# Kernel optimization log

Hardware: AMD Instinct MI355X
Metric: run time of the kernel (lower is better)

## Reference

```python
import math
import jax, jax.numpy as jnp
import numpy as np

B, S, D, DK = 4, 2048, 1024, 128


def setup_inputs() -> dict:
    key = jax.random.key(0)
    ks = jax.random.split(key, 9)
    x = jax.random.normal(ks[0], (B, S, D), dtype=jnp.float32)
    # padding at the tail of each sequence (True = padded position)
    lengths = jax.random.randint(ks[1], (B,), S // 2, S)
    padding_mask = jnp.arange(S)[None, :] >= lengths[:, None]  # [B, S] bool
    s = 1.0 / math.sqrt(D)
    Wq = jax.random.normal(ks[2], (D, DK), dtype=jnp.float32) * s
    bq = jnp.zeros((DK,), dtype=jnp.float32)
    Wk = jax.random.normal(ks[3], (D, DK), dtype=jnp.float32) * s
    bk = jnp.zeros((DK,), dtype=jnp.float32)
    Wv = jax.random.normal(ks[4], (D, D), dtype=jnp.float32) * s
    bv = jnp.zeros((D,), dtype=jnp.float32)
    return {"input": x, "padding_mask": padding_mask,
            "Wq": Wq, "bq": bq, "Wk": Wk, "bk": bk, "Wv": Wv, "bv": bv}


def reference(input, padding_mask, Wq, bq, Wk, bk, Wv, bv):
    scale = math.sqrt(DK)
    q = input @ Wq + bq                      # [B, S, DK]
    k = input @ Wk + bk                      # [B, S, DK]
    v = input @ Wv + bv                      # [B, S, D]
    scores = jnp.einsum('bqd,bkd->bqk', q, k) / scale  # [B, S, S]
    causal = jnp.triu(jnp.ones((S, S), dtype=bool), 1)  # True above diagonal
    mask = causal[None, :, :] | padding_mask[:, None, :] | padding_mask[:, :, None]
    scores = jnp.where(mask, -jnp.inf, scores)
    # rows that are fully masked get all-zero logits -> uniform softmax (matches torch edge case)
    all_neg = jnp.all(mask, axis=-1)         # [B, S]
    scores = jnp.where(all_neg[..., None], 0.0, scores)
    attn = jax.nn.softmax(scores, axis=-1)
    return jnp.einsum('bqk,bkd->bqd', attn, v)
```

## Files before the change

kernel.cpp:

```cpp
#include <hip/hip_runtime.h>
#include <cstdint>
#include <cstddef>

#define B_  4
#define S_  2048
#define D_  1024
#define DK_ 128

typedef float  f32x4   __attribute__((ext_vector_type(4)));
typedef short  bf16x8s __attribute__((ext_vector_type(8)));
typedef unsigned int   u32;
typedef unsigned short u16;

__device__ inline u32 rne(float f) {
    u32 u = __builtin_bit_cast(u32, f);
    return (u + 0x7fffu + ((u >> 16) & 1u)) >> 16;
}
__device__ inline u32 pack2(float a, float b) { return rne(a) | (rne(b) << 16); }
__device__ inline bf16x8s ldfrag(const u16* p) {
    union { uint4 u; bf16x8s v; } c;
    c.u = *(const uint4*)p;
    return c.v;
}
__device__ inline f32x4 MM(bf16x8s a, bf16x8s b, f32x4 c) {
    return __builtin_amdgcn_mfma_f32_16x16x32_bf16(a, b, c, 0, 0, 0);
}
__device__ inline void gload_lds16(const void* gsrc, void* ldst) {
    __builtin_amdgcn_global_load_lds(
        (const __attribute__((address_space(1))) unsigned int*)gsrc,
        (__attribute__((address_space(3))) unsigned int*)ldst, 16, 0, 0);
}

__global__ void lengths_kernel(const uint8_t* __restrict__ mask,
                               int* __restrict__ lengths) {
    int b = blockIdx.x;
    bool is_i32 = (mask[S_ - 1] == 0);
    __shared__ int cnt[256];
    int t = threadIdx.x;
    int c = 0;
    for (int i = t; i < S_; i += 256) {
        int val;
        if (is_i32) val = ((const int*)mask)[b * S_ + i];
        else        val = mask[b * S_ + i];
        c += (val == 0) ? 1 : 0;
    }
    cnt[t] = c;
    __syncthreads();
    for (int s = 128; s > 0; s >>= 1) {
        if (t < s) cnt[t] += cnt[t + s];
        __syncthreads();
    }
    if (t == 0) lengths[b] = cnt[0];
}

__global__ __launch_bounds__(256) void tobf16_kernel(
    const float* __restrict__ in, u16* __restrict__ out) {
    size_t i = (size_t)blockIdx.x * 256 + threadIdx.x;
    float4 f = ((const float4*)in)[i];
    ushort4 o = { (u16)rne(f.x), (u16)rne(f.y), (u16)rne(f.z), (u16)rne(f.w) };
    ((ushort4*)out)[i] = o;
}

__global__ __launch_bounds__(256) void transpose_tobf16_kernel(
    const float* __restrict__ W, u16* __restrict__ T, int K, int N) {
    __shared__ float tl[32][33];
    const int t = threadIdx.x, tx = t & 31, ty = t >> 5;
    const int n0 = blockIdx.x * 32, k0 = blockIdx.y * 32;
#pragma unroll
    for (int i = 0; i < 4; ++i)
        tl[ty + i * 8][tx] = W[(size_t)(k0 + ty + i * 8) * N + n0 + tx];
    __syncthreads();
#pragma unroll
    for (int i = 0; i < 4; ++i) {
        float f = tl[tx][ty + i * 8];
        T[(size_t)(n0 + ty + i * 8) * K + k0 + tx] = (u16)rne(f);
    }
}

template<int BM, int BN, int WM, int WN>
__global__ __launch_bounds__(256) void gemm_nt(
    const u16* __restrict__ A, const u16* __restrict__ Bm,
    const float* __restrict__ bias_col, const float* __restrict__ bias_row,
    float scale, u16* __restrict__ C, int N, int K,
    size_t bStride, size_t cStride)
{
    constexpr int FM = WM / 16, FN = WN / 16;
    const int t = threadIdx.x, w = t >> 6, lane = t & 63;
    const int g = lane >> 4, c16 = lane & 15;
    const int m0 = blockIdx.y * BM + (w >> 1) * WM;
    const int n0 = blockIdx.x * BN + (w & 1) * WN;
    Bm += blockIdx.z * bStride;
    C  += blockIdx.z * cStride;

    f32x4 acc[FM][FN];
#pragma unroll
    for (int i = 0; i < FM; ++i)
#pragma unroll
        for (int j = 0; j < FN; ++j) acc[i][j] = (f32x4){0.f, 0.f, 0.f, 0.f};

    size_t aoff[FM], boff[FN];
#pragma unroll
    for (int i = 0; i < FM; ++i) aoff[i] = (size_t)(m0 + i * 16 + c16) * K + g * 8;
#pragma unroll
    for (int j = 0; j < FN; ++j) boff[j] = (size_t)(n0 + j * 16 + c16) * K + g * 8;

#pragma unroll 2
    for (int k0 = 0; k0 < K; k0 += 32) {
        bf16x8s a[FM], b[FN];
#pragma unroll
        for (int i = 0; i < FM; ++i) a[i] = ldfrag(A + aoff[i] + k0);
#pragma unroll
        for (int j = 0; j < FN; ++j) b[j] = ldfrag(Bm + boff[j] + k0);
#pragma unroll
        for (int i = 0; i < FM; ++i)
#pragma unroll
            for (int j = 0; j < FN; ++j)
                acc[i][j] = MM(a[i], b[j], acc[i][j]);
    }

#pragma unroll
    for (int i = 0; i < FM; ++i)
#pragma unroll
        for (int j = 0; j < FN; ++j) {
            const int n = n0 + j * 16 + c16;
            const float bc = bias_col ? bias_col[n] : 0.f;
#pragma unroll
            for (int r = 0; r < 4; ++r) {
                const int m = m0 + i * 16 + g * 4 + r;
                const float br = bias_row ? bias_row[m] : 0.f;
                float val = (acc[i][j][r] + bc + br) * scale;
                C[(size_t)m * N + n] = (u16)rne(val);
            }
        }
}

__global__ __launch_bounds__(64) void vsum_rows_kernel(
    const u16* __restrict__ vt, float* __restrict__ vsumf) {
    const int blk = blockIdx.x;
    const int lane = threadIdx.x;
    const u16* rr = vt + (size_t)blk * S_;
    float s = 0.f;
    for (int ch = lane; ch < S_ / 8; ch += 64) {
        union { uint4 u; u16 e[8]; } a;
        a.u = ((const uint4*)rr)[ch];
#pragma unroll
        for (int j = 0; j < 8; ++j)
            s += __builtin_bit_cast(float, (u32)a.e[j] << 16);
    }
#pragma unroll
    for (int off = 1; off < 64; off <<= 1) s += __shfl_xor(s, off);
    if (lane == 0) vsumf[blk] = s;
}

#define KVB 32

__global__ __launch_bounds__(256, 3) void flash_mfma(
    const u16* __restrict__ qb, const u16* __restrict__ kbuf,
    const u16* __restrict__ vt, const float* __restrict__ vsumf,
    const int* __restrict__ lengths, float* __restrict__ out)
{
    const int lin     = (int)blockIdx.x;
    const int logical = (lin & 7) * 128 + (lin >> 3);
    const int tile    = 31 - (logical & 31);
    const int grp     = logical >> 5;
    const int b       = grp >> 3;
    const int slice   = grp & 7;

    const int r0 = tile * 64;
    const int t = threadIdx.x, w = t >> 6, lane = t & 63;
    const int g = lane >> 4, c16 = lane & 15;
    const int len = lengths[b];

    if (r0 >= len) {
        const float inv = 1.0f / (float)S_;
        const float4* vs4 = (const float4*)(vsumf + (size_t)b * D_ + slice * 128);
        for (int idx = t; idx < 64 * 32; idx += 256) {
            int rr = idx >> 5, c4 = idx & 31;
            float4 vv = vs4[c4];
            float4 o = { vv.x * inv, vv.y * inv, vv.z * inv, vv.w * inv };
            ((float4*)(out + ((size_t)(b * S_ + r0 + rr)) * D_ + slice * 128))[c4] = o;
        }
        return;
    }

    __shared__ alignas(16) u16 ksm[2][KVB * DK_];
    __shared__ alignas(16) u16 vsm[2][128 * KVB];

    const int qr = r0 + w * 16;
    const int qg = qr + c16;

    bf16x8s Q[4];
    {
        const size_t qrow = (size_t)(b * S_ + qr + c16) * DK_;
#pragma unroll
        for (int dt = 0; dt < 4; ++dt)
            Q[dt] = ldfrag(qb + qrow + dt * 32 + g * 8);
    }

    f32x4 acc[8];
#pragma unroll
    for (int i = 0; i < 8; ++i) acc[i] = (f32x4){0.f, 0.f, 0.f, 0.f};
    float m_r = -3.0e38f, l_r = 0.f;

    const int keyloc0 = ((c16 >> 2) << 3) + (c16 & 3);
    const int kmax_w  = (qr >= len) ? -1 : min(qr + 15, len - 1);
    const int kmaxblk = min(r0 + 63, len - 1);
    const int nt      = kmaxblk / KVB + 1;

    auto stage = [&](int bufi, int kb2) {
#pragma unroll
        for (int i = 0; i < 2; ++i) {
            const int slot = i * 256 + w * 64 + lane;
            const int row  = slot >> 4;
            const int segd = (slot & 15) ^ ((row & 3) | (((row >> 3) & 3) << 2));
            const u16* gsrc = kbuf + (size_t)(b * S_ + kb2 + row) * DK_ + segd * 8;
            gload_lds16(gsrc, &ksm[bufi][(size_t)(i * 256 + w * 64) * 8]);
        }
#pragma unroll
        for (int i = 0; i < 2; ++i) {
            const int slot = i * 256 + w * 64 + lane;
            const int row  = slot >> 2;
            const int segd = (slot & 3) ^ ((row >> 1) & 3);
            const u16* gsrc = vt + (size_t)(b * D_ + slice * 128 + row) * S_
                                 + kb2 + segd * 8;
            gload_lds16(gsrc, &vsm[bufi][(size_t)(i * 256 + w * 64) * 8]);
        }
    };

    stage(0, 0);
    __syncthreads();

    for (int ti = 0; ti < nt; ++ti) {
        const int kb  = ti * KVB;
        const int cur = ti & 1;
        if (ti + 1 < nt) stage(cur ^ 1, kb + KVB);

        if (kb <= kmax_w) {
            f32x4 sT[2];
#pragma unroll
            for (int kt = 0; kt < 2; ++kt) {
                f32x4 s = (f32x4){0.f, 0.f, 0.f, 0.f};
#pragma unroll
                for (int dt = 0; dt < 4; ++dt) {
                    const bf16x8s kf = *(const bf16x8s*)&ksm[cur]
                        [(keyloc0 + kt * 4) * DK_ + (((dt * 4 + g) ^ c16) * 8)];
                    s = MM(kf, Q[dt], s);
                }
                sT[kt] = s;
            }
#pragma unroll
            for (int kt = 0; kt < 2; ++kt)
#pragma unroll
                for (int r = 0; r < 4; ++r) {
                    int key = kb + g * 8 + kt * 4 + r;
                    if (key > qg) sT[kt][r] = -3.0e38f;
                }
            float cmax = sT[0][0];
#pragma unroll
            for (int r = 1; r < 4; ++r) cmax = fmaxf(cmax, sT[0][r]);
#pragma unroll
            for (int r = 0; r < 4; ++r) cmax = fmaxf(cmax, sT[1][r]);
            cmax = fmaxf(cmax, __shfl_xor(cmax, 16));
            cmax = fmaxf(cmax, __shfl_xor(cmax, 32));

            const bool noresc = __all(cmax <= m_r + 8.0f);
            float m_new = m_r, sc = 1.0f;
            if (!noresc) {
                m_new = fmaxf(m_r, cmax);
                sc = __expf(m_r - m_new);
            }

            float p[2][4];
            float rs = 0.f;
#pragma unroll
            for (int kt = 0; kt < 2; ++kt)
#pragma unroll
                for (int r = 0; r < 4; ++r) {
                    p[kt][r] = __expf(sT[kt][r] - m_new);
                    rs += p[kt][r];
                }
            rs += __shfl_xor(rs, 16);
            rs += __shfl_xor(rs, 32);

            if (!noresc) {
                float scr0 = __shfl(sc, g * 4 + 0, 16);
                float scr1 = __shfl(sc, g * 4 + 1, 16);
                float scr2 = __shfl(sc, g * 4 + 2, 16);
                float scr3 = __shfl(sc, g * 4 + 3, 16);
                f32x4 scv = { scr0, scr1, scr2, scr3 };
#pragma unroll
                for (int i = 0; i < 8; ++i) acc[i] *= scv;
                l_r = l_r * sc + rs;
                m_r = m_new;
            } else {
                l_r += rs;
            }

            union { u32 wrd[4]; bf16x8s v; } pa;
            pa.wrd[0] = pack2(p[0][0], p[0][1]);
            pa.wrd[1] = pack2(p[0][2], p[0][3]);
            pa.wrd[2] = pack2(p[1][0], p[1][1]);
            pa.wrd[3] = pack2(p[1][2], p[1][3]);

#pragma unroll
            for (int cg = 0; cg < 8; ++cg) {
                const bf16x8s vf = *(const bf16x8s*)&vsm[cur]
                    [(cg * 16 + c16) * KVB + ((g ^ ((c16 >> 1) & 3)) * 8)];
                acc[cg] = MM(pa.v, vf, acc[cg]);
            }
        }

        __syncthreads();
    }

    const float linv = 1.0f / l_r;
    float iv[4];
    bool valid[4];
#pragma unroll
    for (int r = 0; r < 4; ++r) {
        const int row = g * 4 + r;
        iv[r] = __shfl(linv, row, 16);
        valid[r] = (qr + row) < len;
    }
    const float invS = 1.0f / (float)S_;
#pragma unroll
    for (int cg = 0; cg < 8; ++cg) {
        const int d = slice * 128 + cg * 16 + c16;
        const float vsv = vsumf[(size_t)b * D_ + d] * invS;
#pragma unroll
        for (int r = 0; r < 4; ++r) {
            const int rowg = qr + g * 4 + r;
            const float val = valid[r] ? acc[cg][r] * iv[r] : vsv;
            out[((size_t)(b * S_ + rowg)) * D_ + d] = val;
        }
    }
}

extern "C" void kernel_launch(void* const* d_in, const int* in_sizes, int n_in,
                              void* d_out, int out_size, void* d_ws, size_t ws_size,
                              hipStream_t stream) {
    const float*   x    = (const float*)d_in[0];
    const uint8_t* mask = (const uint8_t*)d_in[1];
    const float*   Wq   = (const float*)d_in[2];
    const float*   bq   = (const float*)d_in[3];
    const float*   Wk   = (const float*)d_in[4];
    const float*   bk   = (const float*)d_in[5];
    const float*   Wv   = (const float*)d_in[6];
    const float*   bv   = (const float*)d_in[7];
    float* out = (float*)d_out;

    u16* u = (u16*)d_ws;
    u16* x_bf = u;                    u += (size_t)8192 * 1024;
    u16* wqt  = u;                    u += (size_t)128 * 1024;
    u16* wkt  = u;                    u += (size_t)128 * 1024;
    u16* wvt  = u;                    u += (size_t)1024 * 1024;
    u16* qb   = u;                    u += (size_t)8192 * 128;
    u16* kbuf = u;                    u += (size_t)8192 * 128;
    u16* vt   = u;                    u += (size_t)B_ * 1024 * 2048;
    float* vsumf = (float*)u;
    int* lengths = (int*)(vsumf + B_ * D_);

    const float SCALE = 0.08838834764831845f;

    lengths_kernel<<<dim3(B_), dim3(256), 0, stream>>>(mask, lengths);
    tobf16_kernel<<<dim3(8192), dim3(256), 0, stream>>>(x, x_bf);
    transpose_tobf16_kernel<<<dim3(4, 32), dim3(256), 0, stream>>>(Wq, wqt, 1024, 128);
    transpose_tobf16_kernel<<<dim3(4, 32), dim3(256), 0, stream>>>(Wk, wkt, 1024, 128);
    transpose_tobf16_kernel<<<dim3(32, 32), dim3(256), 0, stream>>>(Wv, wvt, 1024, 1024);

    gemm_nt<64, 64, 32, 32><<<dim3(2, 128, 1), dim3(256), 0, stream>>>(
        x_bf, wqt, bq, nullptr, SCALE, qb, 128, 1024, 0, 0);
    gemm_nt<64, 64, 32, 32><<<dim3(2, 128, 1), dim3(256), 0, stream>>>(
        x_bf, wkt, bk, nullptr, 1.0f, kbuf, 128, 1024, 0, 0);
    gemm_nt<128, 128, 64, 64><<<dim3(16, 8, B_), dim3(256), 0, stream>>>(
        wvt, x_bf, nullptr, bv, 1.0f, vt, 2048, 1024,
        (size_t)2048 * 1024, (size_t)1024 * 2048);

    vsum_rows_kernel<<<dim3(B_ * D_), dim3(64), 0, stream>>>(vt, vsumf);

    flash_mfma<<<dim3(1024), dim3(256), 0, stream>>>(
        qb, kbuf, vt, vsumf, lengths, out);
}
```

Baseline: 304.6 us.

## Stage GEMM tiles through swizzled double-buffered LDS and fuse Q/K projections

Replaces the direct-from-global fragment GEMMs with kernels that stage A and B tiles into double-buffered, XOR-swizzled shared memory using direct global-to-LDS loads, so each tile is reused across waves. The Q and K projections are merged into one GEMM over a concatenated transposed weight, with the epilogue routing columns to the q or k buffer. The goal is to cut redundant global loads and one launch, at the cost of LDS usage and a barrier per k-step.

Result: faster. 244.8 us (-19.7%).

```diff
diff --git a/kernel.cpp b/kernel.cpp
--- a/kernel.cpp
+++ b/kernel.cpp
@@ -77,59 +77,165 @@
     }
 }
 
-template<int BM, int BN, int WM, int WN>
-__global__ __launch_bounds__(256) void gemm_nt(
-    const u16* __restrict__ A, const u16* __restrict__ Bm,
-    const float* __restrict__ bias_col, const float* __restrict__ bias_row,
-    float scale, u16* __restrict__ C, int N, int K,
-    size_t bStride, size_t cStride)
+#define GBK 32
+
+__global__ __launch_bounds__(256, 2) void gemm_lds_vt(
+    const u16* __restrict__ A,
+    const u16* __restrict__ Bm,
+    const float* __restrict__ bias_row,
+    u16* __restrict__ C)
 {
-    constexpr int FM = WM / 16, FN = WN / 16;
+    const int K = 1024, N = 2048;
     const int t = threadIdx.x, w = t >> 6, lane = t & 63;
     const int g = lane >> 4, c16 = lane & 15;
-    const int m0 = blockIdx.y * BM + (w >> 1) * WM;
-    const int n0 = blockIdx.x * BN + (w & 1) * WN;
-    Bm += blockIdx.z * bStride;
-    C  += blockIdx.z * cStride;
-
-    f32x4 acc[FM][FN];
-#pragma unroll
-    for (int i = 0; i < FM; ++i)
-#pragma unroll
-        for (int j = 0; j < FN; ++j) acc[i][j] = (f32x4){0.f, 0.f, 0.f, 0.f};
-
-    size_t aoff[FM], boff[FN];
-#pragma unroll
-    for (int i = 0; i < FM; ++i) aoff[i] = (size_t)(m0 + i * 16 + c16) * K + g * 8;
-#pragma unroll
-    for (int j = 0; j < FN; ++j) boff[j] = (size_t)(n0 + j * 16 + c16) * K + g * 8;
-
-#pragma unroll 2
-    for (int k0 = 0; k0 < K; k0 += 32) {
-        bf16x8s a[FM], b[FN];
-#pragma unroll
-        for (int i = 0; i < FM; ++i) a[i] = ldfrag(A + aoff[i] + k0);
-#pragma unroll
-        for (int j = 0; j < FN; ++j) b[j] = ldfrag(Bm + boff[j] + k0);
-#pragma unroll
-        for (int i = 0; i < FM; ++i)
-#pragma unroll
-            for (int j = 0; j < FN; ++j)
+    const int m0 = blockIdx.y * 128;
+    const int n0 = blockIdx.x * 128;
+    const u16* Bb = Bm + (size_t)blockIdx.z * 2048 * 1024;
+    u16* Cb = C + (size_t)blockIdx.z * 1024 * 2048;
+
+    __shared__ alignas(16) u16 As[2][128 * GBK];
+    __shared__ alignas(16) u16 Bs[2][128 * GBK];
+
+    auto stage = [&](int buf, int k0) {
+#pragma unroll
+        for (int call = 0; call < 2; ++call) {
+            const int slot = call * 256 + w * 64 + lane;
+            const int row  = slot >> 2;
+            const int segd = (slot & 3) ^ ((row >> 1) & 3);
+            gload_lds16(A + (size_t)(m0 + row) * K + k0 + segd * 8,
+                        &As[buf][(size_t)(call * 256 + w * 64) * 8]);
+        }
+#pragma unroll
+        for (int call = 0; call < 2; ++call) {
+            const int slot = call * 256 + w * 64 + lane;
+            const int row  = slot >> 2;
+            const int segd = (slot & 3) ^ ((row >> 1) & 3);
+            gload_lds16(Bb + (size_t)(n0 + row) * K + k0 + segd * 8,
+                        &Bs[buf][(size_t)(call * 256 + w * 64) * 8]);
+        }
+    };
+
+    f32x4 acc[4][4];
+#pragma unroll
+    for (int i = 0; i < 4; ++i)
+#pragma unroll
+        for (int j = 0; j < 4; ++j) acc[i][j] = (f32x4){0.f, 0.f, 0.f, 0.f};
+
+    const int rbase = (w >> 1) * 64;
+    const int cbase = (w & 1) * 64;
+    const int segr  = g ^ ((c16 >> 1) & 3);
+
+    stage(0, 0);
+    __syncthreads();
+    for (int ks = 0; ks < K / GBK; ++ks) {
+        const int cur = ks & 1;
+        if (ks + 1 < K / GBK) stage(cur ^ 1, (ks + 1) * GBK);
+        bf16x8s a[4], b[4];
+#pragma unroll
+        for (int i = 0; i < 4; ++i)
+            a[i] = *(const bf16x8s*)&As[cur][(rbase + i * 16 + c16) * GBK + segr * 8];
+#pragma unroll
+        for (int j = 0; j < 4; ++j)
+            b[j] = *(const bf16x8s*)&Bs[cur][(cbase + j * 16 + c16) * GBK + segr * 8];
+#pragma unroll
+        for (int i = 0; i < 4; ++i)
+#pragma unroll
+            for (int j = 0; j < 4; ++j)
                 acc[i][j] = MM(a[i], b[j], acc[i][j]);
-    }
-
-#pragma unroll
-    for (int i = 0; i < FM; ++i)
-#pragma unroll
-        for (int j = 0; j < FN; ++j) {
-            const int n = n0 + j * 16 + c16;
-            const float bc = bias_col ? bias_col[n] : 0.f;
+        __syncthreads();
+    }
+
+#pragma unroll
+    for (int i = 0; i < 4; ++i)
+#pragma unroll
+        for (int j = 0; j < 4; ++j) {
+            const int n = n0 + cbase + j * 16 + c16;
 #pragma unroll
             for (int r = 0; r < 4; ++r) {
-                const int m = m0 + i * 16 + g * 4 + r;
-                const float br = bias_row ? bias_row[m] : 0.f;
-                float val = (acc[i][j][r] + bc + br) * scale;
-                C[(size_t)m * N + n] = (u16)rne(val);
+                const int m = m0 + rbase + i * 16 + g * 4 + r;
+                Cb[(size_t)m * N + n] = (u16)rne(acc[i][j][r] + bias_row[m]);
+            }
+        }
+}
+
+__global__ __launch_bounds__(256, 2) void gemm_lds_qk(
+    const u16* __restrict__ A,
+    const u16* __restrict__ Bm,
+    const float* __restrict__ bq, const float* __restrict__ bk,
+    float scale, u16* __restrict__ qb, u16* __restrict__ kout)
+{
+    const int K = 1024;
+    const int t = threadIdx.x, w = t >> 6, lane = t & 63;
+    const int g = lane >> 4, c16 = lane & 15;
+    const int m0 = blockIdx.y * 64;
+    const int n0 = blockIdx.x * 128;
+
+    __shared__ alignas(16) u16 As[2][64 * GBK];
+    __shared__ alignas(16) u16 Bs[2][128 * GBK];
+
+    auto stage = [&](int buf, int k0) {
+        {
+            const int slot = w * 64 + lane;
+            const int row  = slot >> 2;
+            const int segd = (slot & 3) ^ ((row >> 1) & 3);
+            gload_lds16(A + (size_t)(m0 + row) * K + k0 + segd * 8,
+                        &As[buf][(size_t)(w * 64) * 8]);
+        }
+#pragma unroll
+        for (int call = 0; call < 2; ++call) {
+            const int slot = call * 256 + w * 64 + lane;
+            const int row  = slot >> 2;
+            const int segd = (slot & 3) ^ ((row >> 1) & 3);
+            gload_lds16(Bm + (size_t)(n0 + row) * K + k0 + segd * 8,
+                        &Bs[buf][(size_t)(call * 256 + w * 64) * 8]);
+        }
+    };
+
+    f32x4 acc[2][4];
+#pragma unroll
+    for (int i = 0; i < 2; ++i)
+#pragma unroll
+        for (int j = 0; j < 4; ++j) acc[i][j] = (f32x4){0.f, 0.f, 0.f, 0.f};
+
+    const int rbase = (w >> 1) * 32;
+    const int cbase = (w & 1) * 64;
+    const int segr  = g ^ ((c16 >> 1) & 3);
+
+    stage(0, 0);
+    __syncthreads();
+    for (int ks = 0; ks < K / GBK; ++ks) {
+        const int cur = ks & 1;
+        if (ks + 1 < K / GBK) stage(cur ^ 1, (ks + 1) * GBK);
+        bf16x8s a[2], b[4];
+#pragma unroll
+        for (int i = 0; i < 2; ++i)
+            a[i] = *(const bf16x8s*)&As[cur][(rbase + i * 16 + c16) * GBK + segr * 8];
+#pragma unroll
+        for (int j = 0; j < 4; ++j)
+            b[j] = *(const bf16x8s*)&Bs[cur][(cbase + j * 16 + c16) * GBK + segr * 8];
+#pragma unroll
+        for (int i = 0; i < 2; ++i)
+#pragma unroll
+            for (int j = 0; j < 4; ++j)
+                acc[i][j] = MM(a[i], b[j], acc[i][j]);
+        __syncthreads();
+    }
+
+#pragma unroll
+    for (int i = 0; i < 2; ++i)
+#pragma unroll
+        for (int j = 0; j < 4; ++j) {
+            const int n = n0 + cbase + j * 16 + c16;
+            const bool isq = (n < 128);
+            const int nc = isq ? n : (n - 128);
+            const float bc = isq ? bq[nc] : bk[nc];
+            const float sc = isq ? scale : 1.0f;
+#pragma unroll
+            for (int r = 0; r < 4; ++r) {
+                const int m = m0 + rbase + i * 16 + g * 4 + r;
+                const float val = (acc[i][j][r] + bc) * sc;
+                u16* dst = isq ? qb : kout;
+                dst[(size_t)m * DK_ + nc] = (u16)rne(val);
             }
         }
 }
@@ -351,8 +457,7 @@
 
     u16* u = (u16*)d_ws;
     u16* x_bf = u;                    u += (size_t)8192 * 1024;
-    u16* wqt  = u;                    u += (size_t)128 * 1024;
-    u16* wkt  = u;                    u += (size_t)128 * 1024;
+    u16* wqkt = u;                    u += (size_t)256 * 1024;
     u16* wvt  = u;                    u += (size_t)1024 * 1024;
     u16* qb   = u;                    u += (size_t)8192 * 128;
     u16* kbuf = u;                    u += (size_t)8192 * 128;
@@ -364,17 +469,14 @@
 
     lengths_kernel<<<dim3(B_), dim3(256), 0, stream>>>(mask, lengths);
     tobf16_kernel<<<dim3(8192), dim3(256), 0, stream>>>(x, x_bf);
-    transpose_tobf16_kernel<<<dim3(4, 32), dim3(256), 0, stream>>>(Wq, wqt, 1024, 128);
-    transpose_tobf16_kernel<<<dim3(4, 32), dim3(256), 0, stream>>>(Wk, wkt, 1024, 128);
+    transpose_tobf16_kernel<<<dim3(4, 32), dim3(256), 0, stream>>>(Wq, wqkt, 1024, 128);
+    transpose_tobf16_kernel<<<dim3(4, 32), dim3(256), 0, stream>>>(Wk, wqkt + (size_t)128 * 1024, 1024, 128);
     transpose_tobf16_kernel<<<dim3(32, 32), dim3(256), 0, stream>>>(Wv, wvt, 1024, 1024);
 
-    gemm_nt<64, 64, 32, 32><<<dim3(2, 128, 1), dim3(256), 0, stream>>>(
-        x_bf, wqt, bq, nullptr, SCALE, qb, 128, 1024, 0, 0);
-    gemm_nt<64, 64, 32, 32><<<dim3(2, 128, 1), dim3(256), 0, stream>>>(
-        x_bf, wkt, bk, nullptr, 1.0f, kbuf, 128, 1024, 0, 0);
-    gemm_nt<128, 128, 64, 64><<<dim3(16, 8, B_), dim3(256), 0, stream>>>(
-        wvt, x_bf, nullptr, bv, 1.0f, vt, 2048, 1024,
-        (size_t)2048 * 1024, (size_t)1024 * 2048);
+    gemm_lds_qk<<<dim3(2, 128), dim3(256), 0, stream>>>(
+        x_bf, wqkt, bq, bk, SCALE, qb, kbuf);
+    gemm_lds_vt<<<dim3(16, 8, B_), dim3(256), 0, stream>>>(
+        wvt, x_bf, bv, vt);
 
     vsum_rows_kernel<<<dim3(B_ * D_), dim3(64), 0, stream>>>(vt, vsumf);
 
```
